# Kernel tuning notes

Hardware: AMD Instinct MI355X
Metric: run time of the kernel (lower is better)

## Reference

```python
import jax, jax.numpy as jnp
import numpy as np

N_NODES = 200000
N_EDGES = 5000000
N_GRAPHS = 1024
HID = 16
ALPHA = 0.2


def _sage_conv(x, src, dst, Wl, bl, Wr):
    # PyG SAGEConv(aggr='mean'): out = lin_l(mean_{j->i} x_j) + lin_r(x_i)
    msg = x[src]                                                  # [E, d] gather
    summed = jax.ops.segment_sum(msg, dst, num_segments=N_NODES)  # [N, d]
    deg = jax.ops.segment_sum(jnp.ones((src.shape[0],), x.dtype), dst, num_segments=N_NODES)
    mean = summed / jnp.maximum(deg, 1.0)[:, None]
    return mean @ Wl + bl + x @ Wr


def _attention_pool(x, batch):
    scores = jnp.exp(ALPHA * x)                                   # [N, d]
    denom = jax.ops.segment_sum(scores, batch, num_segments=N_GRAPHS)
    scores = scores / denom[batch]
    return jax.ops.segment_sum(x * scores, batch, num_segments=N_GRAPHS)  # [B, d]


def setup_inputs() -> dict:
    key = jax.random.key(0)
    ks = jax.random.split(key, 32)
    inp = {}
    inp['x'] = jax.random.normal(ks[0], (N_NODES, 1), dtype=jnp.float32)
    inp['edge_index'] = jax.random.randint(ks[1], (2, N_EDGES), 0, N_NODES, dtype=jnp.int32)
    inp['batch'] = jnp.sort(jax.random.randint(ks[2], (N_NODES,), 0, N_GRAPHS, dtype=jnp.int32))
    dims = [(1, HID), (HID, HID), (HID, HID)]
    k = 3
    for i, (di, do) in enumerate(dims):
        inp[f'Wl{i}'] = jax.random.normal(ks[k], (di, do), jnp.float32) * 0.1; k += 1
        inp[f'bl{i}'] = jnp.zeros((do,), jnp.float32)
        inp[f'Wr{i}'] = jax.random.normal(ks[k], (di, do), jnp.float32) * 0.1; k += 1
        inp[f'Wlin{i}'] = jax.random.normal(ks[k], (HID, HID), jnp.float32) * 0.1; k += 1
        inp[f'blin{i}'] = jnp.zeros((HID,), jnp.float32)
    inp['Wo0'] = jax.random.normal(ks[k], (HID, HID), jnp.float32) * 0.1; k += 1
    inp['bo0'] = jnp.zeros((HID,), jnp.float32)
    inp['Wo1'] = jax.random.normal(ks[k], (HID, HID), jnp.float32) * 0.1; k += 1
    inp['bo1'] = jnp.zeros((HID,), jnp.float32)
    inp['Wo2'] = jax.random.normal(ks[k], (HID, 1), jnp.float32) * 0.1; k += 1
    inp['bo2'] = jnp.zeros((1,), jnp.float32)
    return inp


def reference(x, edge_index, batch,
              Wl0, bl0, Wr0, Wlin0, blin0,
              Wl1, bl1, Wr1, Wlin1, blin1,
              Wl2, bl2, Wr2, Wlin2, blin2,
              Wo0, bo0, Wo1, bo1, Wo2, bo2):
    src, dst = edge_index[0], edge_index[1]
    Wls = [Wl0, Wl1, Wl2]; bls = [bl0, bl1, bl2]; Wrs = [Wr0, Wr1, Wr2]
    Wlins = [Wlin0, Wlin1, Wlin2]; blins = [blin0, blin1, blin2]
    for i in range(3):
        x = jax.nn.relu(_sage_conv(x, src, dst, Wls[i], bls[i], Wrs[i]))
        x = x @ Wlins[i] + blins[i]
    x = _attention_pool(x, batch)                                 # [B, HID]
    x = jax.nn.relu(x @ Wo0 + bo0)
    x = jax.nn.relu(x @ Wo1 + bo1)
    return x @ Wo2 + bo2                                          # [B, 1]
```

## Files before the change

### kernel.cpp

```cpp
#include <hip/hip_runtime.h>

#define N_NODES 200000
#define N_EDGES 5000000
#define N_GRAPHS 1024
#define HID 16
#define ALPHA 0.2f

#define BSH 7
#define BSZ 128
#define NB 1563
#define NWGB 256
#define EPB ((N_EDGES + NWGB - 1) / NWGB)

#define SACCP 20

__global__ void count_kernel(const int* __restrict__ dst, int* __restrict__ M) {
    __shared__ int hist[NB];
    for (int i = threadIdx.x; i < NB; i += 1024) hist[i] = 0;
    __syncthreads();
    int base = blockIdx.x * EPB;
    int end = min(base + EPB, N_EDGES);
    for (int e = base + threadIdx.x * 4; e < end; e += 1024 * 4) {
        int4 d4 = *reinterpret_cast<const int4*>(dst + e);
        atomicAdd(&hist[d4.x >> BSH], 1);
        atomicAdd(&hist[d4.y >> BSH], 1);
        atomicAdd(&hist[d4.z >> BSH], 1);
        atomicAdd(&hist[d4.w >> BSH], 1);
    }
    __syncthreads();
    for (int i = threadIdx.x; i < NB; i += 1024)
        M[blockIdx.x * NB + i] = hist[i];
}

__global__ void colscan_kernel(int* __restrict__ M, int* __restrict__ col_total) {
    int b = blockIdx.x * blockDim.x + threadIdx.x;
    if (b >= NB) return;
    int run = 0;
#pragma unroll 8
    for (int w = 0; w < NWGB; ++w) {
        int v = M[w * NB + b];
        M[w * NB + b] = run;
        run += v;
    }
    col_total[b] = run;
}

__global__ void bucketscan_kernel(const int* __restrict__ col_total,
                                  int* __restrict__ bucket_base) {
    __shared__ int sc[256];
    int t = threadIdx.x;
    int v[7];
    int s = 0;
#pragma unroll
    for (int k = 0; k < 7; ++k) {
        int i = t * 7 + k;
        v[k] = (i < NB) ? col_total[i] : 0;
        s += v[k];
    }
    sc[t] = s;
    __syncthreads();
    for (int off = 1; off < 256; off <<= 1) {
        int tmp = (t >= off) ? sc[t - off] : 0;
        __syncthreads();
        sc[t] += tmp;
        __syncthreads();
    }
    int excl = sc[t] - s;
#pragma unroll
    for (int k = 0; k < 7; ++k) {
        int i = t * 7 + k;
        if (i < NB) bucket_base[i] = excl;
        excl += v[k];
    }
    if (t == 255) bucket_base[NB] = sc[255];
}

__global__ void scatter_build_kernel(const int* __restrict__ src,
                                     const int* __restrict__ dst,
                                     const int* __restrict__ M,
                                     const int* __restrict__ bucket_base,
                                     int* __restrict__ packed) {
    __shared__ int cur[NB];
    int w = blockIdx.x;
    for (int i = threadIdx.x; i < NB; i += 1024)
        cur[i] = bucket_base[i] + M[w * NB + i];
    __syncthreads();
    int base = w * EPB;
    int end = min(base + EPB, N_EDGES);
    for (int e = base + threadIdx.x * 4; e < end; e += 1024 * 4) {
        int4 s4 = *reinterpret_cast<const int4*>(src + e);
        int4 d4 = *reinterpret_cast<const int4*>(dst + e);
        int p;
        p = atomicAdd(&cur[d4.x >> BSH], 1); packed[p] = (s4.x << BSH) | (d4.x & (BSZ - 1));
        p = atomicAdd(&cur[d4.y >> BSH], 1); packed[p] = (s4.y << BSH) | (d4.y & (BSZ - 1));
        p = atomicAdd(&cur[d4.z >> BSH], 1); packed[p] = (s4.z << BSH) | (d4.z & (BSZ - 1));
        p = atomicAdd(&cur[d4.w >> BSH], 1); packed[p] = (s4.w << BSH) | (d4.w & (BSZ - 1));
    }
}

__global__ void csr_kernel(const int* __restrict__ packed,
                           const int* __restrict__ bucket_base,
                           int* __restrict__ row_ptr,
                           int* __restrict__ sorted_src) {
    __shared__ int cnt[BSZ], scn[BSZ], cur[BSZ];
    int t = threadIdx.x, b = blockIdx.x;
    if (t < BSZ) cnt[t] = 0;
    __syncthreads();
    int e0 = bucket_base[b], e1 = bucket_base[b + 1];
    for (int i = e0 + t; i < e1; i += 256)
        atomicAdd(&cnt[packed[i] & (BSZ - 1)], 1);
    __syncthreads();
    if (t < BSZ) scn[t] = cnt[t];
    __syncthreads();
    for (int off = 1; off < BSZ; off <<= 1) {
        int v = 0;
        if (t < BSZ && t >= off) v = scn[t - off];
        __syncthreads();
        if (t < BSZ) scn[t] += v;
        __syncthreads();
    }
    if (t < BSZ) {
        int node = b * BSZ + t;
        int base = e0 + scn[t] - cnt[t];
        if (node < N_NODES) row_ptr[node] = base;
        cur[t] = base;
    }
    if (b == NB - 1 && t == 0) row_ptr[N_NODES] = N_EDGES;
    __syncthreads();
    for (int i = e0 + t; i < e1; i += 256) {
        int pk = packed[i];
        int p = atomicAdd(&cur[pk & (BSZ - 1)], 1);
        sorted_src[p] = pk >> BSH;
    }
}

__global__ void layer0_csr(const float* __restrict__ x,
                           const int* __restrict__ row_ptr,
                           const int* __restrict__ sorted_src,
                           const float* __restrict__ Wl, const float* __restrict__ bl,
                           const float* __restrict__ Wr,
                           const float* __restrict__ Wlin, const float* __restrict__ blin,
                           float* __restrict__ xout) {
    __shared__ float sWl[HID], sWr[HID], sbl[HID], sblin[HID], sWlin[HID * HID];
    int t = threadIdx.x;
    if (t < HID) {
        sWl[t] = Wl[t]; sWr[t] = Wr[t]; sbl[t] = bl[t]; sblin[t] = blin[t];
    }
    if (t < HID * HID) sWlin[t] = Wlin[t];
    __syncthreads();

    int n = blockIdx.x * 256 + t;
    if (n >= N_NODES) return;
    int r0 = row_ptr[n], r1 = row_ptr[n + 1];
    float sum = 0.0f;
    int i = r0;
    for (; i + 4 <= r1; i += 4) {
        int s0 = sorted_src[i], s1 = sorted_src[i + 1];
        int s2 = sorted_src[i + 2], s3 = sorted_src[i + 3];
        sum += x[s0] + x[s1] + x[s2] + x[s3];
    }
    for (; i < r1; ++i) sum += x[sorted_src[i]];
    float mean = sum / fmaxf((float)(r1 - r0), 1.0f);
    float xv = x[n];
    float h[HID];
#pragma unroll
    for (int j = 0; j < HID; ++j)
        h[j] = fmaxf(mean * sWl[j] + sbl[j] + xv * sWr[j], 0.0f);
    float o[HID];
#pragma unroll
    for (int j = 0; j < HID; ++j) {
        float a = sblin[j];
#pragma unroll
        for (int k = 0; k < HID; ++k) a += h[k] * sWlin[k * HID + j];
        o[j] = a;
    }
    float4* op = reinterpret_cast<float4*>(xout + (size_t)n * HID);
#pragma unroll
    for (int q = 0; q < 4; ++q)
        op[q] = make_float4(o[q * 4 + 0], o[q * 4 + 1], o[q * 4 + 2], o[q * 4 + 3]);
}

__global__ void layerB_csr(const float* __restrict__ xin,
                           const int* __restrict__ row_ptr,
                           const int* __restrict__ sorted_src,
                           const float* __restrict__ Wl, const float* __restrict__ bl,
                           const float* __restrict__ Wr,
                           const float* __restrict__ Wlin, const float* __restrict__ blin,
                           float* __restrict__ xout) {
    __shared__ float sacc[64 * SACCP];
    __shared__ float sxv[64 * SACCP];
    __shared__ float sh[64 * SACCP];
    __shared__ float sWl[HID * HID], sWr[HID * HID], sWlin[HID * HID];
    __shared__ float sbl[HID], sblin[HID];
    int t = threadIdx.x;
    if (t < HID * HID) { sWl[t] = Wl[t]; sWr[t] = Wr[t]; sWlin[t] = Wlin[t]; }
    if (t < HID) { sbl[t] = bl[t]; sblin[t] = blin[t]; }
    __syncthreads();

    int q = t & 3;
    int g = t >> 2;
    int n = blockIdx.x * 64 + g;

    if (n < N_NODES) {
        int r0 = row_ptr[n], r1 = row_ptr[n + 1];
        const float* xq = xin + 4 * q;
        float4 acc = make_float4(0.0f, 0.0f, 0.0f, 0.0f);
        int i = r0;
        for (; i + 8 <= r1; i += 8) {
            int s0 = sorted_src[i],     s1 = sorted_src[i + 1];
            int s2 = sorted_src[i + 2], s3 = sorted_src[i + 3];
            int s4 = sorted_src[i + 4], s5 = sorted_src[i + 5];
            int s6 = sorted_src[i + 6], s7 = sorted_src[i + 7];
            float4 g0 = *reinterpret_cast<const float4*>(xq + (size_t)s0 * HID);
            float4 g1 = *reinterpret_cast<const float4*>(xq + (size_t)s1 * HID);
            float4 g2 = *reinterpret_cast<const float4*>(xq + (size_t)s2 * HID);
            float4 g3 = *reinterpret_cast<const float4*>(xq + (size_t)s3 * HID);
            float4 g4 = *reinterpret_cast<const float4*>(xq + (size_t)s4 * HID);
            float4 g5 = *reinterpret_cast<const float4*>(xq + (size_t)s5 * HID);
            float4 g6 = *reinterpret_cast<const float4*>(xq + (size_t)s6 * HID);
            float4 g7 = *reinterpret_cast<const float4*>(xq + (size_t)s7 * HID);
            acc.x += (g0.x + g1.x + g2.x + g3.x) + (g4.x + g5.x + g6.x + g7.x);
            acc.y += (g0.y + g1.y + g2.y + g3.y) + (g4.y + g5.y + g6.y + g7.y);
            acc.z += (g0.z + g1.z + g2.z + g3.z) + (g4.z + g5.z + g6.z + g7.z);
            acc.w += (g0.w + g1.w + g2.w + g3.w) + (g4.w + g5.w + g6.w + g7.w);
        }
        for (; i + 4 <= r1; i += 4) {
            int s0 = sorted_src[i],     s1 = sorted_src[i + 1];
            int s2 = sorted_src[i + 2], s3 = sorted_src[i + 3];
            float4 g0 = *reinterpret_cast<const float4*>(xq + (size_t)s0 * HID);
            float4 g1 = *reinterpret_cast<const float4*>(xq + (size_t)s1 * HID);
            float4 g2 = *reinterpret_cast<const float4*>(xq + (size_t)s2 * HID);
            float4 g3 = *reinterpret_cast<const float4*>(xq + (size_t)s3 * HID);
            acc.x += g0.x + g1.x + g2.x + g3.x;
            acc.y += g0.y + g1.y + g2.y + g3.y;
            acc.z += g0.z + g1.z + g2.z + g3.z;
            acc.w += g0.w + g1.w + g2.w + g3.w;
        }
        for (; i < r1; ++i) {
            float4 gv = *reinterpret_cast<const float4*>(xq + (size_t)sorted_src[i] * HID);
            acc.x += gv.x; acc.y += gv.y; acc.z += gv.z; acc.w += gv.w;
        }
        float invd = 1.0f / fmaxf((float)(r1 - r0), 1.0f);
        acc.x *= invd; acc.y *= invd; acc.z *= invd; acc.w *= invd;
        *reinterpret_cast<float4*>(&sacc[g * SACCP + 4 * q]) = acc;
        *reinterpret_cast<float4*>(&sxv[g * SACCP + 4 * q]) =
            *reinterpret_cast<const float4*>(xin + (size_t)n * HID + 4 * q);
    }
    __syncthreads();

    if (n < N_NODES) {
        float h4[4];
#pragma unroll
        for (int jj = 0; jj < 4; ++jj) {
            int j = 4 * q + jj;
            float a = sbl[j];
#pragma unroll
            for (int k = 0; k < HID; ++k)
                a += sacc[g * SACCP + k] * sWl[k * HID + j]
                   + sxv[g * SACCP + k] * sWr[k * HID + j];
            h4[jj] = fmaxf(a, 0.0f);
        }
        *reinterpret_cast<float4*>(&sh[g * SACCP + 4 * q]) =
            make_float4(h4[0], h4[1], h4[2], h4[3]);
    }
    __syncthreads();

    if (n < N_NODES) {
        float o4[4];
#pragma unroll
        for (int jj = 0; jj < 4; ++jj) {
            int j = 4 * q + jj;
            float a = sblin[j];
#pragma unroll
            for (int k = 0; k < HID; ++k) a += sh[g * SACCP + k] * sWlin[k * HID + j];
            o4[jj] = a;
        }
        *reinterpret_cast<float4*>(xout + (size_t)n * HID + 4 * q) =
            make_float4(o4[0], o4[1], o4[2], o4[3]);
    }
}

__global__ void scatter0_kernel(const float* __restrict__ x,
                                const int* __restrict__ src,
                                const int* __restrict__ dst,
                                float* __restrict__ sum0,
                                float* __restrict__ deg) {
    int stride = gridDim.x * blockDim.x;
    for (int e = blockIdx.x * blockDim.x + threadIdx.x; e < N_EDGES; e += stride) {
        atomicAdd(&sum0[dst[e]], x[src[e]]);
        atomicAdd(&deg[dst[e]], 1.0f);
    }
}

__global__ void scatter16_kernel(const float* __restrict__ x,
                                 const int* __restrict__ src,
                                 const int* __restrict__ dst,
                                 float* __restrict__ summed) {
    int stride = gridDim.x * blockDim.x;
    const int total = N_EDGES * HID;
    for (int t = blockIdx.x * blockDim.x + threadIdx.x; t < total; t += stride) {
        int e = t >> 4, j = t & 15;
        atomicAdd(&summed[dst[e] * HID + j], x[src[e] * HID + j]);
    }
}

__global__ void node0_kernel(const float* __restrict__ x,
                             const float* __restrict__ sum0,
                             const float* __restrict__ deg,
                             const float* __restrict__ Wl, const float* __restrict__ bl,
                             const float* __restrict__ Wr,
                             const float* __restrict__ Wlin, const float* __restrict__ blin,
                             float* __restrict__ xout) {
    __shared__ float sWl[HID], sWr[HID], sbl[HID], sblin[HID], sWlin[HID * HID];
    if (threadIdx.x < HID) {
        sWl[threadIdx.x] = Wl[threadIdx.x]; sWr[threadIdx.x] = Wr[threadIdx.x];
        sbl[threadIdx.x] = bl[threadIdx.x]; sblin[threadIdx.x] = blin[threadIdx.x];
    }
    if (threadIdx.x < HID * HID) sWlin[threadIdx.x] = Wlin[threadIdx.x];
    __syncthreads();
    int stride = gridDim.x * blockDim.x;
    for (int n = blockIdx.x * blockDim.x + threadIdx.x; n < N_NODES; n += stride) {
        float mean = sum0[n] / fmaxf(deg[n], 1.0f);
        float xv = x[n];
        float h[HID];
#pragma unroll
        for (int j = 0; j < HID; ++j)
            h[j] = fmaxf(mean * sWl[j] + sbl[j] + xv * sWr[j], 0.0f);
#pragma unroll
        for (int j = 0; j < HID; ++j) {
            float acc = sblin[j];
#pragma unroll
            for (int k = 0; k < HID; ++k) acc += h[k] * sWlin[k * HID + j];
            xout[n * HID + j] = acc;
        }
    }
}

__global__ void node16_kernel(const float* __restrict__ xin,
                              const float* __restrict__ sums,
                              const float* __restrict__ deg,
                              const float* __restrict__ Wl, const float* __restrict__ bl,
                              const float* __restrict__ Wr,
                              const float* __restrict__ Wlin, const float* __restrict__ blin,
                              float* __restrict__ xout) {
    __shared__ float sWl[HID * HID], sWr[HID * HID], sWlin[HID * HID];
    __shared__ float sbl[HID], sblin[HID];
    if (threadIdx.x < HID * HID) {
        sWl[threadIdx.x] = Wl[threadIdx.x]; sWr[threadIdx.x] = Wr[threadIdx.x];
        sWlin[threadIdx.x] = Wlin[threadIdx.x];
    }
    if (threadIdx.x < HID) { sbl[threadIdx.x] = bl[threadIdx.x]; sblin[threadIdx.x] = blin[threadIdx.x]; }
    __syncthreads();
    int stride = gridDim.x * blockDim.x;
    for (int n = blockIdx.x * blockDim.x + threadIdx.x; n < N_NODES; n += stride) {
        float invd = 1.0f / fmaxf(deg[n], 1.0f);
        float m[HID], xv[HID];
        const float4* sp = reinterpret_cast<const float4*>(sums + (size_t)n * HID);
        const float4* xp = reinterpret_cast<const float4*>(xin + (size_t)n * HID);
#pragma unroll
        for (int qq = 0; qq < 4; ++qq) {
            float4 sv = sp[qq]; float4 vv = xp[qq];
            m[qq * 4 + 0] = sv.x * invd; m[qq * 4 + 1] = sv.y * invd;
            m[qq * 4 + 2] = sv.z * invd; m[qq * 4 + 3] = sv.w * invd;
            xv[qq * 4 + 0] = vv.x; xv[qq * 4 + 1] = vv.y; xv[qq * 4 + 2] = vv.z; xv[qq * 4 + 3] = vv.w;
        }
        float h[HID];
#pragma unroll
        for (int j = 0; j < HID; ++j) {
            float a = sbl[j];
#pragma unroll
            for (int k = 0; k < HID; ++k) a += m[k] * sWl[k * HID + j];
#pragma unroll
            for (int k = 0; k < HID; ++k) a += xv[k] * sWr[k * HID + j];
            h[j] = fmaxf(a, 0.0f);
        }
        float o[HID];
#pragma unroll
        for (int j = 0; j < HID; ++j) {
            float a = sblin[j];
#pragma unroll
            for (int k = 0; k < HID; ++k) a += h[k] * sWlin[k * HID + j];
            o[j] = a;
        }
        float4* op = reinterpret_cast<float4*>(xout + (size_t)n * HID);
#pragma unroll
        for (int qq = 0; qq < 4; ++qq)
            op[qq] = make_float4(o[qq * 4 + 0], o[qq * 4 + 1], o[qq * 4 + 2], o[qq * 4 + 3]);
    }
}

__global__ void pool_head_kernel(const float* __restrict__ x,
                                 const int* __restrict__ batch,
                                 const float* __restrict__ Wo0, const float* __restrict__ bo0,
                                 const float* __restrict__ Wo1, const float* __restrict__ bo1,
                                 const float* __restrict__ Wo2, const float* __restrict__ bo2,
                                 float* __restrict__ out) {
    int g = blockIdx.x;
    __shared__ int sRange[2];
    __shared__ float red_d[256], red_n[256];
    __shared__ float pooled[HID], h0[HID], h1[HID];

    if (threadIdx.x == 0) {
        int lo = 0, hi = N_NODES;
        while (lo < hi) { int mid = (lo + hi) >> 1; if (batch[mid] < g) lo = mid + 1; else hi = mid; }
        sRange[0] = lo;
        hi = N_NODES;
        while (lo < hi) { int mid = (lo + hi) >> 1; if (batch[mid] < g + 1) lo = mid + 1; else hi = mid; }
        sRange[1] = lo;
    }
    __syncthreads();
    int start = sRange[0], end = sRange[1];
    int j = threadIdx.x & 15;
    int sub = threadIdx.x >> 4;

    float dacc = 0.0f, nacc = 0.0f;
    for (int n = start + sub; n < end; n += 16) {
        float v = x[n * HID + j];
        float s = expf(ALPHA * v);
        dacc += s;
        nacc += s * v;
    }
    red_d[threadIdx.x] = dacc;
    red_n[threadIdx.x] = nacc;
    __syncthreads();

    if (threadIdx.x < HID) {
        float ds = 0.0f, ns = 0.0f;
        for (int k = 0; k < 16; ++k) {
            ds += red_d[k * 16 + threadIdx.x];
            ns += red_n[k * 16 + threadIdx.x];
        }
        pooled[threadIdx.x] = ds > 0.0f ? ns / ds : 0.0f;
    }
    __syncthreads();
    if (threadIdx.x < HID) {
        float acc = bo0[threadIdx.x];
        for (int k = 0; k < HID; ++k) acc += pooled[k] * Wo0[k * HID + threadIdx.x];
        h0[threadIdx.x] = fmaxf(acc, 0.0f);
    }
    __syncthreads();
    if (threadIdx.x < HID) {
        float acc = bo1[threadIdx.x];
        for (int k = 0; k < HID; ++k) acc += h0[k] * Wo1[k * HID + threadIdx.x];
        h1[threadIdx.x] = fmaxf(acc, 0.0f);
    }
    __syncthreads();
    if (threadIdx.x == 0) {
        float acc = bo2[0];
        for (int k = 0; k < HID; ++k) acc += h1[k] * Wo2[k];
        out[g] = acc;
    }
}

extern "C" void kernel_launch(void* const* d_in, const int* in_sizes, int n_in,
                              void* d_out, int out_size, void* d_ws, size_t ws_size,
                              hipStream_t stream) {
    const float* x      = (const float*)d_in[0];
    const int*   edge   = (const int*)d_in[1];
    const int*   batch  = (const int*)d_in[2];
    const float* Wl0    = (const float*)d_in[3];
    const float* bl0    = (const float*)d_in[4];
    const float* Wr0    = (const float*)d_in[5];
    const float* Wlin0  = (const float*)d_in[6];
    const float* blin0  = (const float*)d_in[7];
    const float* Wl1    = (const float*)d_in[8];
    const float* bl1    = (const float*)d_in[9];
    const float* Wr1    = (const float*)d_in[10];
    const float* Wlin1  = (const float*)d_in[11];
    const float* blin1  = (const float*)d_in[12];
    const float* Wl2    = (const float*)d_in[13];
    const float* bl2    = (const float*)d_in[14];
    const float* Wr2    = (const float*)d_in[15];
    const float* Wlin2  = (const float*)d_in[16];
    const float* blin2  = (const float*)d_in[17];
    const float* Wo0    = (const float*)d_in[18];
    const float* bo0    = (const float*)d_in[19];
    const float* Wo1    = (const float*)d_in[20];
    const float* bo1    = (const float*)d_in[21];
    const float* Wo2    = (const float*)d_in[22];
    const float* bo2    = (const float*)d_in[23];

    const int* src = edge;
    const int* dst = edge + N_EDGES;

    const size_t OFF_SORTED = 0;
    const size_t OFF_ROW    = 20000000;
    const size_t OFF_M      = 20800016;
    const size_t OFF_XA     = 22400528;
    const size_t OFF_XB     = 35200528;
    const size_t NEED_MAIN  = 48000528;
    const size_t OFF_PACKED = OFF_XA;
    const size_t OFF_CT     = 42400528;
    const size_t OFF_BB     = 42406800;

    char* ws = (char*)d_ws;

    if (ws_size >= NEED_MAIN) {
        int*   sorted_src  = (int*)(ws + OFF_SORTED);
        int*   row_ptr     = (int*)(ws + OFF_ROW);
        int*   M           = (int*)(ws + OFF_M);
        float* xa          = (float*)(ws + OFF_XA);
        float* xb          = (float*)(ws + OFF_XB);
        int*   packed      = (int*)(ws + OFF_PACKED);
        int*   col_total   = (int*)(ws + OFF_CT);
        int*   bucket_base = (int*)(ws + OFF_BB);

        count_kernel<<<NWGB, 1024, 0, stream>>>(dst, M);
        colscan_kernel<<<(NB + 255) / 256, 256, 0, stream>>>(M, col_total);
        bucketscan_kernel<<<1, 256, 0, stream>>>(col_total, bucket_base);
        scatter_build_kernel<<<NWGB, 1024, 0, stream>>>(src, dst, M, bucket_base, packed);
        csr_kernel<<<NB, 256, 0, stream>>>(packed, bucket_base, row_ptr, sorted_src);

        layer0_csr<<<(N_NODES + 255) / 256, 256, 0, stream>>>(
            x, row_ptr, sorted_src, Wl0, bl0, Wr0, Wlin0, blin0, xa);
        layerB_csr<<<(N_NODES + 63) / 64, 256, 0, stream>>>(
            xa, row_ptr, sorted_src, Wl1, bl1, Wr1, Wlin1, blin1, xb);
        layerB_csr<<<(N_NODES + 63) / 64, 256, 0, stream>>>(
            xb, row_ptr, sorted_src, Wl2, bl2, Wr2, Wlin2, blin2, xa);

        pool_head_kernel<<<N_GRAPHS, 256, 0, stream>>>(xa, batch, Wo0, bo0, Wo1, bo1,
                                                       Wo2, bo2, (float*)d_out);
    } else {
        float* deg    = (float*)ws;
        float* summed = deg + N_NODES;
        float* xa     = summed + (size_t)N_NODES * HID;
        float* xb     = xa + (size_t)N_NODES * HID;

        hipMemsetAsync(deg, 0, sizeof(float) * (size_t)N_NODES * (1 + HID), stream);
        scatter0_kernel<<<2048, 256, 0, stream>>>(x, src, dst, summed, deg);
        node0_kernel<<<784, 256, 0, stream>>>(x, summed, deg, Wl0, bl0, Wr0, Wlin0, blin0, xa);

        hipMemsetAsync(summed, 0, sizeof(float) * (size_t)N_NODES * HID, stream);
        scatter16_kernel<<<4096, 256, 0, stream>>>(xa, src, dst, summed);
        node16_kernel<<<784, 256, 0, stream>>>(xa, summed, deg, Wl1, bl1, Wr1, Wlin1, blin1, xb);

        hipMemsetAsync(summed, 0, sizeof(float) * (size_t)N_NODES * HID, stream);
        scatter16_kernel<<<4096, 256, 0, stream>>>(xb, src, dst, summed);
        node16_kernel<<<784, 256, 0, stream>>>(xb, summed, deg, Wl2, bl2, Wr2, Wlin2, blin2, xa);

        pool_head_kernel<<<N_GRAPHS, 256, 0, stream>>>(xa, batch, Wo0, bo0, Wo1, bo1,
                                                       Wo2, bo2, (float*)d_out);
    }
}
```

Measured before the change: 501.1 us.

## Fuse layer-0 aggregation into CSR build and sort edges in place

```diff
diff --git a/kernel.cpp b/kernel.cpp
--- a/kernel.cpp
+++ b/kernel.cpp
@@ -11,6 +11,7 @@
 #define NB 1563
 #define NWGB 256
 #define EPB ((N_EDGES + NWGB - 1) / NWGB)
+#define ECAP 4096
 
 #define SACCP 20
 
@@ -98,17 +99,34 @@
     }
 }
 
-__global__ void csr_kernel(const int* __restrict__ packed,
-                           const int* __restrict__ bucket_base,
-                           int* __restrict__ row_ptr,
-                           int* __restrict__ sorted_src) {
+__global__ void csr_fused_kernel(const float* __restrict__ x,
+                                 const int* __restrict__ packed,
+                                 const int* __restrict__ bucket_base,
+                                 const float* __restrict__ Wl, const float* __restrict__ bl,
+                                 const float* __restrict__ Wr,
+                                 const float* __restrict__ Wlin, const float* __restrict__ blin,
+                                 int* __restrict__ row_ptr,
+                                 int* sorted_src,
+                                 float* __restrict__ xout) {
+    __shared__ int sEdge[ECAP];
     __shared__ int cnt[BSZ], scn[BSZ], cur[BSZ];
+    __shared__ float ssum[BSZ];
+    __shared__ float sWl[HID], sWr[HID], sbl[HID], sblin[HID], sWlin[HID * HID];
     int t = threadIdx.x, b = blockIdx.x;
-    if (t < BSZ) cnt[t] = 0;
-    __syncthreads();
+    if (t < BSZ) { cnt[t] = 0; ssum[t] = 0.0f; }
+    if (t < HID) { sWl[t] = Wl[t]; sWr[t] = Wr[t]; sbl[t] = bl[t]; sblin[t] = blin[t]; }
+    if (t < HID * HID) sWlin[t] = Wlin[t];
+    __syncthreads();
+
     int e0 = bucket_base[b], e1 = bucket_base[b + 1];
-    for (int i = e0 + t; i < e1; i += 256)
-        atomicAdd(&cnt[packed[i] & (BSZ - 1)], 1);
+    for (int i = e0 + t; i < e1; i += 256) {
+        int pk = packed[i];
+        int off = i - e0;
+        if (off < ECAP) sEdge[off] = pk;
+        int dl = pk & (BSZ - 1);
+        atomicAdd(&cnt[dl], 1);
+        atomicAdd(&ssum[dl], x[pk >> BSH]);
+    }
     __syncthreads();
     if (t < BSZ) scn[t] = cnt[t];
     __syncthreads();
@@ -119,65 +137,42 @@
         if (t < BSZ) scn[t] += v;
         __syncthreads();
     }
+    int node = b * BSZ + t;
     if (t < BSZ) {
-        int node = b * BSZ + t;
         int base = e0 + scn[t] - cnt[t];
         if (node < N_NODES) row_ptr[node] = base;
         cur[t] = base;
     }
     if (b == NB - 1 && t == 0) row_ptr[N_NODES] = N_EDGES;
     __syncthreads();
+
     for (int i = e0 + t; i < e1; i += 256) {
-        int pk = packed[i];
+        int off = i - e0;
+        int pk = (off < ECAP) ? sEdge[off] : packed[i];
         int p = atomicAdd(&cur[pk & (BSZ - 1)], 1);
         sorted_src[p] = pk >> BSH;
     }
-}
-
-__global__ void layer0_csr(const float* __restrict__ x,
-                           const int* __restrict__ row_ptr,
-                           const int* __restrict__ sorted_src,
-                           const float* __restrict__ Wl, const float* __restrict__ bl,
-                           const float* __restrict__ Wr,
-                           const float* __restrict__ Wlin, const float* __restrict__ blin,
-                           float* __restrict__ xout) {
-    __shared__ float sWl[HID], sWr[HID], sbl[HID], sblin[HID], sWlin[HID * HID];
-    int t = threadIdx.x;
-    if (t < HID) {
-        sWl[t] = Wl[t]; sWr[t] = Wr[t]; sbl[t] = bl[t]; sblin[t] = blin[t];
-    }
-    if (t < HID * HID) sWlin[t] = Wlin[t];
-    __syncthreads();
-
-    int n = blockIdx.x * 256 + t;
-    if (n >= N_NODES) return;
-    int r0 = row_ptr[n], r1 = row_ptr[n + 1];
-    float sum = 0.0f;
-    int i = r0;
-    for (; i + 4 <= r1; i += 4) {
-        int s0 = sorted_src[i], s1 = sorted_src[i + 1];
-        int s2 = sorted_src[i + 2], s3 = sorted_src[i + 3];
-        sum += x[s0] + x[s1] + x[s2] + x[s3];
-    }
-    for (; i < r1; ++i) sum += x[sorted_src[i]];
-    float mean = sum / fmaxf((float)(r1 - r0), 1.0f);
-    float xv = x[n];
-    float h[HID];
-#pragma unroll
-    for (int j = 0; j < HID; ++j)
-        h[j] = fmaxf(mean * sWl[j] + sbl[j] + xv * sWr[j], 0.0f);
-    float o[HID];
-#pragma unroll
-    for (int j = 0; j < HID; ++j) {
-        float a = sblin[j];
-#pragma unroll
-        for (int k = 0; k < HID; ++k) a += h[k] * sWlin[k * HID + j];
-        o[j] = a;
-    }
-    float4* op = reinterpret_cast<float4*>(xout + (size_t)n * HID);
-#pragma unroll
-    for (int q = 0; q < 4; ++q)
-        op[q] = make_float4(o[q * 4 + 0], o[q * 4 + 1], o[q * 4 + 2], o[q * 4 + 3]);
+
+    if (t < BSZ && node < N_NODES) {
+        float mean = ssum[t] / fmaxf((float)cnt[t], 1.0f);
+        float xv = x[node];
+        float h[HID];
+#pragma unroll
+        for (int j = 0; j < HID; ++j)
+            h[j] = fmaxf(mean * sWl[j] + sbl[j] + xv * sWr[j], 0.0f);
+        float o[HID];
+#pragma unroll
+        for (int j = 0; j < HID; ++j) {
+            float a = sblin[j];
+#pragma unroll
+            for (int k = 0; k < HID; ++k) a += h[k] * sWlin[k * HID + j];
+            o[j] = a;
+        }
+        float4* op = reinterpret_cast<float4*>(xout + (size_t)node * HID);
+#pragma unroll
+        for (int q = 0; q < 4; ++q)
+            op[q] = make_float4(o[q * 4 + 0], o[q * 4 + 1], o[q * 4 + 2], o[q * 4 + 3]);
+    }
 }
 
 __global__ void layerB_csr(const float* __restrict__ xin,
@@ -489,19 +484,18 @@
     const size_t OFF_XA     = 22400528;
     const size_t OFF_XB     = 35200528;
     const size_t NEED_MAIN  = 48000528;
-    const size_t OFF_PACKED = OFF_XA;
     const size_t OFF_CT     = 42400528;
     const size_t OFF_BB     = 42406800;
 
     char* ws = (char*)d_ws;
 
     if (ws_size >= NEED_MAIN) {
-        int*   sorted_src  = (int*)(ws + OFF_SORTED);
+        int*   packed      = (int*)(ws + OFF_SORTED);
+        int*   sorted_src  = packed;
         int*   row_ptr     = (int*)(ws + OFF_ROW);
         int*   M           = (int*)(ws + OFF_M);
         float* xa          = (float*)(ws + OFF_XA);
         float* xb          = (float*)(ws + OFF_XB);
-        int*   packed      = (int*)(ws + OFF_PACKED);
         int*   col_total   = (int*)(ws + OFF_CT);
         int*   bucket_base = (int*)(ws + OFF_BB);
 
@@ -509,10 +503,10 @@
         colscan_kernel<<<(NB + 255) / 256, 256, 0, stream>>>(M, col_total);
         bucketscan_kernel<<<1, 256, 0, stream>>>(col_total, bucket_base);
         scatter_build_kernel<<<NWGB, 1024, 0, stream>>>(src, dst, M, bucket_base, packed);
-        csr_kernel<<<NB, 256, 0, stream>>>(packed, bucket_base, row_ptr, sorted_src);
-
-        layer0_csr<<<(N_NODES + 255) / 256, 256, 0, stream>>>(
-            x, row_ptr, sorted_src, Wl0, bl0, Wr0, Wlin0, blin0, xa);
+        csr_fused_kernel<<<NB, 256, 0, stream>>>(x, packed, bucket_base,
+                                                 Wl0, bl0, Wr0, Wlin0, blin0,
+                                                 row_ptr, sorted_src, xa);
+
         layerB_csr<<<(N_NODES + 63) / 64, 256, 0, stream>>>(
             xa, row_ptr, sorted_src, Wl1, bl1, Wr1, Wlin1, blin1, xb);
         layerB_csr<<<(N_NODES + 63) / 64, 256, 0, stream>>>(
```

New measurement: 476.4 us. -4.9%, faster.
